# Kernel optimization log

Hardware: AMD Instinct MI355X
Metric: run time of the kernel (lower is better)

## Reference

```python
import jax, jax.numpy as jnp
import numpy as np

H = 1024   # hidden_size
V = 32000  # output_size (vocab)
B = 64     # batch
S = 2048   # encoder seq_len


def setup_inputs() -> dict:
    key = jax.random.key(0)
    ks = jax.random.split(key, 12)
    sc = 0.02
    return {
        "input_seq": jax.random.randint(ks[0], (B,), 0, V),
        "last_hidden": jax.random.normal(ks[1], (1, B, H), jnp.float32),
        "encoder_outputs": jax.random.normal(ks[2], (S, B, H), jnp.float32),
        "emb": jax.random.normal(ks[3], (V, H), jnp.float32) * sc,
        "w_ih": jax.random.normal(ks[4], (3 * H, H), jnp.float32) * sc,
        "w_hh": jax.random.normal(ks[5], (3 * H, H), jnp.float32) * sc,
        "b_ih": jnp.zeros((3 * H,), jnp.float32),
        "b_hh": jnp.zeros((3 * H,), jnp.float32),
        "attn_w": jax.random.normal(ks[6], (H, H), jnp.float32) * sc,
        "attn_b": jnp.zeros((H,), jnp.float32),
        "concat_w": jax.random.normal(ks[7], (H, 2 * H), jnp.float32) * sc,
        "concat_b": jnp.zeros((H,), jnp.float32),
        "out_w": jax.random.normal(ks[8], (V, H), jnp.float32) * sc,
        "out_b": jnp.zeros((V,), jnp.float32),
    }


def _forward(input_seq, last_hidden, encoder_outputs, emb, w_ih, w_hh, b_ih, b_hh,
             attn_w, attn_b, concat_w, concat_b, out_w, out_b):
    # 1. embedding (dropout = identity in eval)
    x = emb[input_seq]                      # [b, h]
    h = last_hidden[0]                      # [b, h]
    # 2. single-step GRU (PyTorch gate order: reset, update, new)
    gx = x @ w_ih.T + b_ih                  # [b, 3h]
    gh = h @ w_hh.T + b_hh                  # [b, 3h]
    r = jax.nn.sigmoid(gx[:, :H] + gh[:, :H])
    z = jax.nn.sigmoid(gx[:, H:2 * H] + gh[:, H:2 * H])
    n = jnp.tanh(gx[:, 2 * H:] + r * gh[:, 2 * H:])
    h_new = (1.0 - z) * n + z * h           # [b, h] = rnn_output
    # 3. Luong 'general' attention: score = y . (W enc + b)
    proj = jnp.einsum('sbh,gh->sbg', encoder_outputs, attn_w) + attn_b  # [s,b,h]
    scores = jnp.einsum('bh,sbh->bs', h_new, proj)                      # [b,s]
    attn_weights = jax.nn.softmax(scores, axis=-1)                      # [b,s]
    # 4. context = weights bmm encoder_outputs
    context = jnp.einsum('bs,sbh->bh', attn_weights, encoder_outputs)   # [b,h]
    # 5. concat -> linear -> tanh -> out
    cat = jnp.concatenate([h_new, context], axis=-1)                    # [b,2h]
    concat_output = jnp.tanh(cat @ concat_w.T + concat_b)               # [b,h]
    output = concat_output @ out_w.T + out_b                            # [b,V]
    return output, h_new[None], attn_weights[:, None, :]


def reference(input_seq, last_hidden, encoder_outputs, emb, w_ih, w_hh, b_ih, b_hh,
              attn_w, attn_b, concat_w, concat_b, out_w, out_b):
    return _forward(input_seq, last_hidden, encoder_outputs, emb, w_ih, w_hh, b_ih,
                    b_hh, attn_w, attn_b, concat_w, concat_b, out_w, out_b)
```

## Files before the change

kernel.cpp:

```cpp
#include <hip/hip_runtime.h>

#define HS 1024
#define VS 32000
#define BS 64
#define SS 2048
#define NCH 64
#define SCH (SS/NCH)

typedef __attribute__((ext_vector_type(4))) float f4v;
typedef __attribute__((ext_vector_type(8))) short s8v;

__device__ __forceinline__ float sigmf(float x) { return 1.0f / (1.0f + __expf(-x)); }

__device__ __forceinline__ short bf16c(float f) {
  unsigned u = __builtin_bit_cast(unsigned, f);
  u = (u + 0x7FFFu + ((u >> 16) & 1u)) >> 16;
  return (short)u;
}

__global__ __launch_bounds__(256) void k_prep(const int* __restrict__ idx,
    const float* __restrict__ emb, const float* __restrict__ hid,
    const float* __restrict__ aw,
    short* __restrict__ fx, short* __restrict__ fh, short* __restrict__ awf) {
  int t = blockIdx.x * 256 + threadIdx.x;
  {
    int lane = t & 63, nt = (t >> 6) & 63, kt = t >> 12;
    int kr = kt * 32 + ((lane >> 4) & 3) * 8;
    int col = nt * 16 + (lane & 15);
    const float* sp = aw + (size_t)kr * HS + col;
    s8v v;
#pragma unroll
    for (int j = 0; j < 8; j++) v[j] = bf16c(sp[(size_t)j * HS]);
    *(s8v*)(awf + (size_t)t * 8) = v;
  }
  if (t < 8192) {
    int lane = t & 63, ct = (t >> 6) & 3, kt = t >> 8;
    int col = ct * 16 + (lane & 15);
    int kr = kt * 32 + ((lane >> 4) & 3) * 8;
    const float* sp = emb + (size_t)idx[col] * HS + kr;
    s8v v;
#pragma unroll
    for (int j = 0; j < 8; j++) v[j] = bf16c(sp[j]);
    *(s8v*)(fx + (size_t)t * 8) = v;
  } else if (t < 16384) {
    int t2 = t - 8192;
    int lane = t2 & 63, ct = (t2 >> 6) & 3, kt = t2 >> 8;
    int col = ct * 16 + (lane & 15);
    int kr = kt * 32 + ((lane >> 4) & 3) * 8;
    const float* sp = hid + (size_t)col * HS + kr;
    s8v v;
#pragma unroll
    for (int j = 0; j < 8; j++) v[j] = bf16c(sp[j]);
    *(s8v*)(fh + (size_t)t2 * 8) = v;
  }
}

template<int K, int OL>
__global__ __launch_bounds__(256) void mfsk(
    const float* __restrict__ W0, const short* __restrict__ xf0,
    const float* __restrict__ bias0, void* __restrict__ dst0,
    const float* __restrict__ W1, const short* __restrict__ xf1,
    const float* __restrict__ bias1, void* __restrict__ dst1) {
  const float* W    = blockIdx.y ? W1 : W0;
  const short* xf   = blockIdx.y ? xf1 : xf0;
  const float* bias = blockIdx.y ? bias1 : bias0;
  void* dst         = blockIdx.y ? dst1 : dst0;
  int lane = threadIdx.x & 63;
  int ks = threadIdx.x >> 6;
  int mt = blockIdx.x;
  int row = mt * 16 + (lane & 15);
  const int KW = (K / 32) / 4;
  const float* wp = W + (size_t)row * K + ((lane >> 4) * 8);
  const s8v* xp = (const s8v*)xf + lane;
  f4v acc0 = {0,0,0,0}, acc1 = {0,0,0,0}, acc2 = {0,0,0,0}, acc3 = {0,0,0,0};
#pragma unroll 4
  for (int kk = 0; kk < KW; kk++) {
    int kt = ks * KW + kk;
    float4 wa = *(const float4*)(wp + (size_t)kt * 32);
    float4 wb = *(const float4*)(wp + (size_t)kt * 32 + 4);
    s8v a;
    a[0] = bf16c(wa.x); a[1] = bf16c(wa.y); a[2] = bf16c(wa.z); a[3] = bf16c(wa.w);
    a[4] = bf16c(wb.x); a[5] = bf16c(wb.y); a[6] = bf16c(wb.z); a[7] = bf16c(wb.w);
    const s8v* xk = xp + (size_t)kt * 256;
    acc0 = __builtin_amdgcn_mfma_f32_16x16x32_bf16(a, xk[0],   acc0, 0, 0, 0);
    acc1 = __builtin_amdgcn_mfma_f32_16x16x32_bf16(a, xk[64],  acc1, 0, 0, 0);
    acc2 = __builtin_amdgcn_mfma_f32_16x16x32_bf16(a, xk[128], acc2, 0, 0, 0);
    acc3 = __builtin_amdgcn_mfma_f32_16x16x32_bf16(a, xk[192], acc3, 0, 0, 0);
  }
  __shared__ float red[4][4][4][64];
#pragma unroll
  for (int r = 0; r < 4; r++) {
    red[ks][0][r][lane] = acc0[r];
    red[ks][1][r][lane] = acc1[r];
    red[ks][2][r][lane] = acc2[r];
    red[ks][3][r][lane] = acc3[r];
  }
  __syncthreads();
  int ct = ks;
  int rr0 = mt * 16 + (lane >> 4) * 4;
  int col = ct * 16 + (lane & 15);
#pragma unroll
  for (int r = 0; r < 4; r++) {
    float v = red[0][ct][r][lane] + red[1][ct][r][lane] +
              red[2][ct][r][lane] + red[3][ct][r][lane] + bias[rr0 + r];
    if (OL == 0)
      ((float*)dst)[(size_t)(rr0 + r) * BS + col] = v;
    else
      ((short*)dst)[(size_t)col * HS + rr0 + r] = bf16c(tanhf(v));
  }
}

__global__ __launch_bounds__(256) void k_hnew(const float* __restrict__ gxt,
    const float* __restrict__ ght, const float* __restrict__ hid,
    float* __restrict__ out_h, short* __restrict__ fcat) {
  int tid = blockIdx.x * 256 + threadIdx.x;
  int b = tid & 63, i = tid >> 6;
  float r = sigmf(gxt[i * BS + b] + ght[i * BS + b]);
  float z = sigmf(gxt[(HS + i) * BS + b] + ght[(HS + i) * BS + b]);
  float n = tanhf(gxt[(2 * HS + i) * BS + b] + r * ght[(2 * HS + i) * BS + b]);
  float hn = (1.0f - z) * n + z * hid[(size_t)b * HS + i];
  out_h[(size_t)b * HS + i] = hn;
  int kt = i >> 5, j = i & 7;
  int lane = (b & 15) | (((i >> 3) & 3) << 4);
  int ct = b >> 4;
  fcat[((size_t)((kt * 4 + ct) * 64 + lane)) * 8 + j] = bf16c(hn);
}

__global__ __launch_bounds__(256) void k_qgemm(const float* __restrict__ hnr,
    const short* __restrict__ awf, float* __restrict__ qrow) {
  int lane = threadIdx.x & 63;
  int mt = threadIdx.x >> 6;
  int nt = blockIdx.x;
  const float* ap = hnr + (size_t)(mt * 16 + (lane & 15)) * HS + ((lane >> 4) * 8);
  const s8v* bp = (const s8v*)awf + (size_t)nt * 64 + lane;
  f4v acc = {0,0,0,0};
#pragma unroll 4
  for (int kt = 0; kt < 32; kt++) {
    float4 wa = *(const float4*)(ap + kt * 32);
    float4 wb = *(const float4*)(ap + kt * 32 + 4);
    s8v a;
    a[0] = bf16c(wa.x); a[1] = bf16c(wa.y); a[2] = bf16c(wa.z); a[3] = bf16c(wa.w);
    a[4] = bf16c(wb.x); a[5] = bf16c(wb.y); a[6] = bf16c(wb.z); a[7] = bf16c(wb.w);
    acc = __builtin_amdgcn_mfma_f32_16x16x32_bf16(a, bp[(size_t)kt * 4096], acc, 0, 0, 0);
  }
  int r0 = mt * 16 + (lane >> 4) * 4;
  int hcol = nt * 16 + (lane & 15);
#pragma unroll
  for (int r = 0; r < 4; r++)
    qrow[(size_t)(r0 + r) * HS + hcol] = acc[r];
}

__global__ __launch_bounds__(256, 4) void k_attn(const float* __restrict__ enc,
    const float* __restrict__ qrow, float* __restrict__ scores,
    float* __restrict__ mch, float* __restrict__ lch, float* __restrict__ ctxp) {
  int lane = threadIdx.x & 63;
  int w = blockIdx.x * 4 + (threadIdx.x >> 6);
  int b = w & 63;
  int ch = w >> 6;
  const float* qb = qrow + (size_t)b * HS + lane * 4;
  float4 q0 = *(const float4*)(qb + 0);
  float4 q1 = *(const float4*)(qb + 256);
  float4 q2 = *(const float4*)(qb + 512);
  float4 q3 = *(const float4*)(qb + 768);
  int s0 = ch * SCH;
  const float* ep = enc + ((size_t)s0 * BS + b) * HS + lane * 4;
  float4 e0 = *(const float4*)(ep + 0);
  float4 e1 = *(const float4*)(ep + 256);
  float4 e2 = *(const float4*)(ep + 512);
  float4 e3 = *(const float4*)(ep + 768);
  float m = -1e30f, l = 0.f;
  float4 a0 = {0,0,0,0}, a1 = {0,0,0,0}, a2 = {0,0,0,0}, a3 = {0,0,0,0};
  for (int si = 0; si < SCH; si++) {
    float4 c0 = e0, c1 = e1, c2 = e2, c3 = e3;
    if (si + 1 < SCH) {
      const float* np = ep + (size_t)BS * HS;
      e0 = *(const float4*)(np + 0);
      e1 = *(const float4*)(np + 256);
      e2 = *(const float4*)(np + 512);
      e3 = *(const float4*)(np + 768);
    }
    ep += (size_t)BS * HS;
    float d0 = fmaf(c0.x,q0.x, fmaf(c0.y,q0.y, fmaf(c0.z,q0.z, c0.w*q0.w)));
    float d1 = fmaf(c1.x,q1.x, fmaf(c1.y,q1.y, fmaf(c1.z,q1.z, c1.w*q1.w)));
    float d2 = fmaf(c2.x,q2.x, fmaf(c2.y,q2.y, fmaf(c2.z,q2.z, c2.w*q2.w)));
    float d3 = fmaf(c3.x,q3.x, fmaf(c3.y,q3.y, fmaf(c3.z,q3.z, c3.w*q3.w)));
    float p = (d0 + d1) + (d2 + d3);
#pragma unroll
    for (int off = 32; off; off >>= 1) p += __shfl_xor(p, off, 64);
    if (lane == 0) scores[(size_t)b * SS + s0 + si] = p;
    float mn = fmaxf(m, p);
    float sc = __expf(m - mn);
    float pr = __expf(p - mn);
    l = fmaf(l, sc, pr);
    a0.x = fmaf(a0.x, sc, pr * c0.x); a0.y = fmaf(a0.y, sc, pr * c0.y);
    a0.z = fmaf(a0.z, sc, pr * c0.z); a0.w = fmaf(a0.w, sc, pr * c0.w);
    a1.x = fmaf(a1.x, sc, pr * c1.x); a1.y = fmaf(a1.y, sc, pr * c1.y);
    a1.z = fmaf(a1.z, sc, pr * c1.z); a1.w = fmaf(a1.w, sc, pr * c1.w);
    a2.x = fmaf(a2.x, sc, pr * c2.x); a2.y = fmaf(a2.y, sc, pr * c2.y);
    a2.z = fmaf(a2.z, sc, pr * c2.z); a2.w = fmaf(a2.w, sc, pr * c2.w);
    a3.x = fmaf(a3.x, sc, pr * c3.x); a3.y = fmaf(a3.y, sc, pr * c3.y);
    a3.z = fmaf(a3.z, sc, pr * c3.z); a3.w = fmaf(a3.w, sc, pr * c3.w);
    m = mn;
  }
  if (lane == 0) { mch[b * NCH + ch] = m; lch[b * NCH + ch] = l; }
  float* cp = ctxp + ((size_t)(b * NCH + ch)) * HS + lane * 4;
  *(float4*)(cp + 0)   = a0;
  *(float4*)(cp + 256) = a1;
  *(float4*)(cp + 512) = a2;
  *(float4*)(cp + 768) = a3;
}

__global__ __launch_bounds__(256) void k_combine(const float* __restrict__ mch,
    const float* __restrict__ lch, const float* __restrict__ ctxp,
    const float* __restrict__ scores, short* __restrict__ fcat,
    float* __restrict__ wout) {
  int b = blockIdx.x;
  int t = threadIdx.x;
  __shared__ float sm[NCH], sl[NCH], ssc[NCH];
  if (t < NCH) { sm[t] = mch[b * NCH + t]; sl[t] = lch[b * NCH + t]; }
  __syncthreads();
  float mstar = -1e30f;
  for (int c = 0; c < NCH; c++) mstar = fmaxf(mstar, sm[c]);
  if (t < NCH) ssc[t] = __expf(sm[t] - mstar);
  __syncthreads();
  float L = 0.f;
  for (int c = 0; c < NCH; c++) L = fmaf(sl[c], ssc[c], L);
  float invL = 1.0f / L;
  int h = blockIdx.y * 256 + t;
  float acc = 0.f;
  for (int c = 0; c < NCH; c++)
    acc = fmaf(ctxp[((size_t)(b * NCH + c)) * HS + h], ssc[c], acc);
  float ctx = acc * invL;
  int kc = HS + h;
  int kt = kc >> 5, j = kc & 7;
  int lane2 = (b & 15) | (((kc >> 3) & 3) << 4);
  int ct = b >> 4;
  fcat[((size_t)((kt * 4 + ct) * 64 + lane2)) * 8 + j] = bf16c(ctx);
  if (blockIdx.y == 0)
    for (int s = t; s < SS; s += 256)
      wout[(size_t)b * SS + s] = __expf(scores[(size_t)b * SS + s] - mstar) * invL;
}

__global__ __launch_bounds__(256) void k_out2(const short* __restrict__ cbf,
    const float* __restrict__ ow, const float* __restrict__ ob,
    float* __restrict__ out0) {
  int lane = threadIdx.x & 63;
  int wv = threadIdx.x >> 6;
  int nt = blockIdx.x * 4 + wv;
  int v0 = nt * 16;
  const float* wp = ow + (size_t)(v0 + (lane & 15)) * HS + ((lane >> 4) * 8);
  const short* a0p = cbf + (size_t)(0  + (lane & 15)) * HS + ((lane >> 4) * 8);
  const short* a1p = a0p + (size_t)16 * HS;
  const short* a2p = a0p + (size_t)32 * HS;
  const short* a3p = a0p + (size_t)48 * HS;
  f4v acc0 = {0,0,0,0}, acc1 = {0,0,0,0}, acc2 = {0,0,0,0}, acc3 = {0,0,0,0};
#pragma unroll 4
  for (int kt = 0; kt < 32; kt++) {
    float4 wa = *(const float4*)(wp + kt * 32);
    float4 wb = *(const float4*)(wp + kt * 32 + 4);
    s8v bf;
    bf[0] = bf16c(wa.x); bf[1] = bf16c(wa.y); bf[2] = bf16c(wa.z); bf[3] = bf16c(wa.w);
    bf[4] = bf16c(wb.x); bf[5] = bf16c(wb.y); bf[6] = bf16c(wb.z); bf[7] = bf16c(wb.w);
    s8v fa0 = *(const s8v*)(a0p + kt * 32);
    s8v fa1 = *(const s8v*)(a1p + kt * 32);
    s8v fa2 = *(const s8v*)(a2p + kt * 32);
    s8v fa3 = *(const s8v*)(a3p + kt * 32);
    acc0 = __builtin_amdgcn_mfma_f32_16x16x32_bf16(fa0, bf, acc0, 0, 0, 0);
    acc1 = __builtin_amdgcn_mfma_f32_16x16x32_bf16(fa1, bf, acc1, 0, 0, 0);
    acc2 = __builtin_amdgcn_mfma_f32_16x16x32_bf16(fa2, bf, acc2, 0, 0, 0);
    acc3 = __builtin_amdgcn_mfma_f32_16x16x32_bf16(fa3, bf, acc3, 0, 0, 0);
  }
  float bv = ob[v0 + (lane & 15)];
  int rb = (lane >> 4) * 4;
  int vc = v0 + (lane & 15);
#pragma unroll
  for (int r = 0; r < 4; r++) {
    out0[(size_t)(0  + rb + r) * VS + vc] = acc0[r] + bv;
    out0[(size_t)(16 + rb + r) * VS + vc] = acc1[r] + bv;
    out0[(size_t)(32 + rb + r) * VS + vc] = acc2[r] + bv;
    out0[(size_t)(48 + rb + r) * VS + vc] = acc3[r] + bv;
  }
}

extern "C" void kernel_launch(void* const* d_in, const int* in_sizes, int n_in,
                              void* d_out, int out_size, void* d_ws, size_t ws_size,
                              hipStream_t stream) {
  const int*   idx  = (const int*)d_in[0];
  const float* hid  = (const float*)d_in[1];
  const float* enc  = (const float*)d_in[2];
  const float* emb  = (const float*)d_in[3];
  const float* w_ih = (const float*)d_in[4];
  const float* w_hh = (const float*)d_in[5];
  const float* b_ih = (const float*)d_in[6];
  const float* b_hh = (const float*)d_in[7];
  const float* aw   = (const float*)d_in[8];
  const float* cw   = (const float*)d_in[10];
  const float* cb   = (const float*)d_in[11];
  const float* ow   = (const float*)d_in[12];
  const float* ob   = (const float*)d_in[13];

  float* out0  = (float*)d_out;
  float* out_h = out0 + (size_t)BS * VS;
  float* out_w = out_h + (size_t)BS * HS;

  float* ws   = (float*)d_ws;
  float* gxt  = ws;
  float* ght  = gxt + (size_t)3 * HS * BS;
  float* qrow = ght + (size_t)3 * HS * BS;
  float* scr  = qrow + (size_t)HS * BS;
  float* mch  = scr + (size_t)BS * SS;
  float* lch  = mch + (size_t)BS * NCH;
  float* ctxp = lch + (size_t)BS * NCH;
  short* awf  = (short*)(ctxp + (size_t)BS * NCH * HS);
  short* fx   = awf + (size_t)HS * HS;
  short* fh   = fx  + (size_t)HS * BS;
  short* fcat = fh  + (size_t)HS * BS;
  short* cbf  = fcat + (size_t)2 * HS * BS;

  k_prep   <<<dim3(512), dim3(256), 0, stream>>>(idx, emb, hid, aw, fx, fh, awf);
  mfsk<HS, 0><<<dim3(3 * HS / 16, 2), dim3(256), 0, stream>>>(
      w_ih, fx, b_ih, gxt, w_hh, fh, b_hh, ght);
  k_hnew   <<<dim3(HS * BS / 256), dim3(256), 0, stream>>>(gxt, ght, hid, out_h, fcat);
  k_qgemm  <<<dim3(HS / 16), dim3(256), 0, stream>>>(out_h, awf, qrow);
  k_attn   <<<dim3(BS * NCH / 4), dim3(256), 0, stream>>>(enc, qrow, scr, mch, lch, ctxp);
  k_combine<<<dim3(BS, 4), dim3(256), 0, stream>>>(mch, lch, ctxp, scr, fcat, out_w);
  mfsk<2 * HS, 1><<<dim3(HS / 16, 1), dim3(256), 0, stream>>>(
      cw, fcat, cb, cbf, cw, fcat, cb, cbf);
  k_out2   <<<dim3(VS / 64), dim3(256), 0, stream>>>(cbf, ow, ob, out0);
}
```

Before: 210.4 us.

## Fuse prep conversion into GRU gate GEMM, drop awf pre-pack, double-buffer attention loads

Removes the k_prep kernel. The GRU gate GEMM now gathers embedding and hidden rows directly and converts them to bf16 in-register, summing the K-split partials through shared memory. k_qgemm reads the fp32 attention weight with strided column loads instead of a pre-packed bf16 layout. The attention loop keeps two encoder rows in flight to deepen prefetch. This saves one launch and the pack traffic, at the cost of redundant conversions and poorly coalesced strided loads in k_qgemm.

```diff
diff --git a/kernel.cpp b/kernel.cpp
--- a/kernel.cpp
+++ b/kernel.cpp
@@ -18,53 +18,80 @@
   return (short)u;
 }
 
-__global__ __launch_bounds__(256) void k_prep(const int* __restrict__ idx,
-    const float* __restrict__ emb, const float* __restrict__ hid,
-    const float* __restrict__ aw,
-    short* __restrict__ fx, short* __restrict__ fh, short* __restrict__ awf) {
-  int t = blockIdx.x * 256 + threadIdx.x;
-  {
-    int lane = t & 63, nt = (t >> 6) & 63, kt = t >> 12;
-    int kr = kt * 32 + ((lane >> 4) & 3) * 8;
-    int col = nt * 16 + (lane & 15);
-    const float* sp = aw + (size_t)kr * HS + col;
-    s8v v;
-#pragma unroll
-    for (int j = 0; j < 8; j++) v[j] = bf16c(sp[(size_t)j * HS]);
-    *(s8v*)(awf + (size_t)t * 8) = v;
-  }
-  if (t < 8192) {
-    int lane = t & 63, ct = (t >> 6) & 3, kt = t >> 8;
+__global__ __launch_bounds__(256) void k_gatesf(
+    const int* __restrict__ idx, const float* __restrict__ emb,
+    const float* __restrict__ hid,
+    const float* __restrict__ w_ih, const float* __restrict__ w_hh,
+    const float* __restrict__ b_ih, const float* __restrict__ b_hh,
+    float* __restrict__ gxt, float* __restrict__ ght) {
+  int y = blockIdx.y;
+  const float* W    = y ? w_hh : w_ih;
+  const float* bias = y ? b_hh : b_ih;
+  float* dst        = y ? ght : gxt;
+  int lane = threadIdx.x & 63;
+  int ks = threadIdx.x >> 6;
+  int mt = blockIdx.x;
+  int row = mt * 16 + (lane & 15);
+  const float* wp = W + (size_t)row * HS + ((lane >> 4) * 8);
+  const float* rp[4];
+#pragma unroll
+  for (int ct = 0; ct < 4; ct++) {
     int col = ct * 16 + (lane & 15);
-    int kr = kt * 32 + ((lane >> 4) & 3) * 8;
-    const float* sp = emb + (size_t)idx[col] * HS + kr;
-    s8v v;
-#pragma unroll
-    for (int j = 0; j < 8; j++) v[j] = bf16c(sp[j]);
-    *(s8v*)(fx + (size_t)t * 8) = v;
-  } else if (t < 16384) {
-    int t2 = t - 8192;
-    int lane = t2 & 63, ct = (t2 >> 6) & 3, kt = t2 >> 8;
-    int col = ct * 16 + (lane & 15);
-    int kr = kt * 32 + ((lane >> 4) & 3) * 8;
-    const float* sp = hid + (size_t)col * HS + kr;
-    s8v v;
-#pragma unroll
-    for (int j = 0; j < 8; j++) v[j] = bf16c(sp[j]);
-    *(s8v*)(fh + (size_t)t2 * 8) = v;
+    rp[ct] = y ? (hid + (size_t)col * HS) : (emb + (size_t)idx[col] * HS);
+  }
+  f4v acc0 = {0,0,0,0}, acc1 = {0,0,0,0}, acc2 = {0,0,0,0}, acc3 = {0,0,0,0};
+#pragma unroll 4
+  for (int kk = 0; kk < 8; kk++) {
+    int kt = ks * 8 + kk;
+    int kr = kt * 32 + ((lane >> 4) * 8);
+    float4 wa = *(const float4*)(wp + (size_t)kt * 32);
+    float4 wb = *(const float4*)(wp + (size_t)kt * 32 + 4);
+    s8v a;
+    a[0] = bf16c(wa.x); a[1] = bf16c(wa.y); a[2] = bf16c(wa.z); a[3] = bf16c(wa.w);
+    a[4] = bf16c(wb.x); a[5] = bf16c(wb.y); a[6] = bf16c(wb.z); a[7] = bf16c(wb.w);
+    float4 xa, xb;
+    s8v bf;
+    xa = *(const float4*)(rp[0] + kr); xb = *(const float4*)(rp[0] + kr + 4);
+    bf[0] = bf16c(xa.x); bf[1] = bf16c(xa.y); bf[2] = bf16c(xa.z); bf[3] = bf16c(xa.w);
+    bf[4] = bf16c(xb.x); bf[5] = bf16c(xb.y); bf[6] = bf16c(xb.z); bf[7] = bf16c(xb.w);
+    acc0 = __builtin_amdgcn_mfma_f32_16x16x32_bf16(a, bf, acc0, 0, 0, 0);
+    xa = *(const float4*)(rp[1] + kr); xb = *(const float4*)(rp[1] + kr + 4);
+    bf[0] = bf16c(xa.x); bf[1] = bf16c(xa.y); bf[2] = bf16c(xa.z); bf[3] = bf16c(xa.w);
+    bf[4] = bf16c(xb.x); bf[5] = bf16c(xb.y); bf[6] = bf16c(xb.z); bf[7] = bf16c(xb.w);
+    acc1 = __builtin_amdgcn_mfma_f32_16x16x32_bf16(a, bf, acc1, 0, 0, 0);
+    xa = *(const float4*)(rp[2] + kr); xb = *(const float4*)(rp[2] + kr + 4);
+    bf[0] = bf16c(xa.x); bf[1] = bf16c(xa.y); bf[2] = bf16c(xa.z); bf[3] = bf16c(xa.w);
+    bf[4] = bf16c(xb.x); bf[5] = bf16c(xb.y); bf[6] = bf16c(xb.z); bf[7] = bf16c(xb.w);
+    acc2 = __builtin_amdgcn_mfma_f32_16x16x32_bf16(a, bf, acc2, 0, 0, 0);
+    xa = *(const float4*)(rp[3] + kr); xb = *(const float4*)(rp[3] + kr + 4);
+    bf[0] = bf16c(xa.x); bf[1] = bf16c(xa.y); bf[2] = bf16c(xa.z); bf[3] = bf16c(xa.w);
+    bf[4] = bf16c(xb.x); bf[5] = bf16c(xb.y); bf[6] = bf16c(xb.z); bf[7] = bf16c(xb.w);
+    acc3 = __builtin_amdgcn_mfma_f32_16x16x32_bf16(a, bf, acc3, 0, 0, 0);
+  }
+  __shared__ float red[4][4][4][64];
+#pragma unroll
+  for (int r = 0; r < 4; r++) {
+    red[ks][0][r][lane] = acc0[r];
+    red[ks][1][r][lane] = acc1[r];
+    red[ks][2][r][lane] = acc2[r];
+    red[ks][3][r][lane] = acc3[r];
+  }
+  __syncthreads();
+  int ct = ks;
+  int rr0 = mt * 16 + (lane >> 4) * 4;
+  int col = ct * 16 + (lane & 15);
+#pragma unroll
+  for (int r = 0; r < 4; r++) {
+    float v = red[0][ct][r][lane] + red[1][ct][r][lane] +
+              red[2][ct][r][lane] + red[3][ct][r][lane] + bias[rr0 + r];
+    dst[(size_t)(rr0 + r) * BS + col] = v;
   }
 }
 
 template<int K, int OL>
 __global__ __launch_bounds__(256) void mfsk(
-    const float* __restrict__ W0, const short* __restrict__ xf0,
-    const float* __restrict__ bias0, void* __restrict__ dst0,
-    const float* __restrict__ W1, const short* __restrict__ xf1,
-    const float* __restrict__ bias1, void* __restrict__ dst1) {
-  const float* W    = blockIdx.y ? W1 : W0;
-  const short* xf   = blockIdx.y ? xf1 : xf0;
-  const float* bias = blockIdx.y ? bias1 : bias0;
-  void* dst         = blockIdx.y ? dst1 : dst0;
+    const float* __restrict__ W, const short* __restrict__ xf,
+    const float* __restrict__ bias, void* __restrict__ dst) {
   int lane = threadIdx.x & 63;
   int ks = threadIdx.x >> 6;
   int mt = blockIdx.x;
@@ -127,12 +154,12 @@
 }
 
 __global__ __launch_bounds__(256) void k_qgemm(const float* __restrict__ hnr,
-    const short* __restrict__ awf, float* __restrict__ qrow) {
+    const float* __restrict__ aw, float* __restrict__ qrow) {
   int lane = threadIdx.x & 63;
   int mt = threadIdx.x >> 6;
   int nt = blockIdx.x;
   const float* ap = hnr + (size_t)(mt * 16 + (lane & 15)) * HS + ((lane >> 4) * 8);
-  const s8v* bp = (const s8v*)awf + (size_t)nt * 64 + lane;
+  const float* awc = aw + nt * 16 + (lane & 15);
   f4v acc = {0,0,0,0};
 #pragma unroll 4
   for (int kt = 0; kt < 32; kt++) {
@@ -141,7 +168,12 @@
     s8v a;
     a[0] = bf16c(wa.x); a[1] = bf16c(wa.y); a[2] = bf16c(wa.z); a[3] = bf16c(wa.w);
     a[4] = bf16c(wb.x); a[5] = bf16c(wb.y); a[6] = bf16c(wb.z); a[7] = bf16c(wb.w);
-    acc = __builtin_amdgcn_mfma_f32_16x16x32_bf16(a, bp[(size_t)kt * 4096], acc, 0, 0, 0);
+    int kr = kt * 32 + ((lane >> 4) * 8);
+    const float* bp = awc + (size_t)kr * HS;
+    s8v bfr;
+#pragma unroll
+    for (int j = 0; j < 8; j++) bfr[j] = bf16c(bp[(size_t)j * HS]);
+    acc = __builtin_amdgcn_mfma_f32_16x16x32_bf16(a, bfr, acc, 0, 0, 0);
   }
   int r0 = mt * 16 + (lane >> 4) * 4;
   int hcol = nt * 16 + (lane & 15);
@@ -163,44 +195,82 @@
   float4 q2 = *(const float4*)(qb + 512);
   float4 q3 = *(const float4*)(qb + 768);
   int s0 = ch * SCH;
+  const size_t sstr = (size_t)BS * HS;
   const float* ep = enc + ((size_t)s0 * BS + b) * HS + lane * 4;
-  float4 e0 = *(const float4*)(ep + 0);
-  float4 e1 = *(const float4*)(ep + 256);
-  float4 e2 = *(const float4*)(ep + 512);
-  float4 e3 = *(const float4*)(ep + 768);
+  float4 eA0 = *(const float4*)(ep + 0);
+  float4 eA1 = *(const float4*)(ep + 256);
+  float4 eA2 = *(const float4*)(ep + 512);
+  float4 eA3 = *(const float4*)(ep + 768);
+  const float* ep1 = ep + sstr;
+  float4 eB0 = *(const float4*)(ep1 + 0);
+  float4 eB1 = *(const float4*)(ep1 + 256);
+  float4 eB2 = *(const float4*)(ep1 + 512);
+  float4 eB3 = *(const float4*)(ep1 + 768);
   float m = -1e30f, l = 0.f;
   float4 a0 = {0,0,0,0}, a1 = {0,0,0,0}, a2 = {0,0,0,0}, a3 = {0,0,0,0};
-  for (int si = 0; si < SCH; si++) {
-    float4 c0 = e0, c1 = e1, c2 = e2, c3 = e3;
-    if (si + 1 < SCH) {
-      const float* np = ep + (size_t)BS * HS;
-      e0 = *(const float4*)(np + 0);
-      e1 = *(const float4*)(np + 256);
-      e2 = *(const float4*)(np + 512);
-      e3 = *(const float4*)(np + 768);
+  for (int si = 0; si < SCH; si += 2) {
+    {
+      float4 c0 = eA0, c1 = eA1, c2 = eA2, c3 = eA3;
+      if (si + 2 < SCH) {
+        const float* np = ep + (size_t)(si + 2) * sstr;
+        eA0 = *(const float4*)(np + 0);
+        eA1 = *(const float4*)(np + 256);
+        eA2 = *(const float4*)(np + 512);
+        eA3 = *(const float4*)(np + 768);
+      }
+      float d0 = fmaf(c0.x,q0.x, fmaf(c0.y,q0.y, fmaf(c0.z,q0.z, c0.w*q0.w)));
+      float d1 = fmaf(c1.x,q1.x, fmaf(c1.y,q1.y, fmaf(c1.z,q1.z, c1.w*q1.w)));
+      float d2 = fmaf(c2.x,q2.x, fmaf(c2.y,q2.y, fmaf(c2.z,q2.z, c2.w*q2.w)));
+      float d3 = fmaf(c3.x,q3.x, fmaf(c3.y,q3.y, fmaf(c3.z,q3.z, c3.w*q3.w)));
+      float p = (d0 + d1) + (d2 + d3);
+#pragma unroll
+      for (int off = 32; off; off >>= 1) p += __shfl_xor(p, off, 64);
+      if (lane == 0) scores[(size_t)b * SS + s0 + si] = p;
+      float mn = fmaxf(m, p);
+      float sc = __expf(m - mn);
+      float pr = __expf(p - mn);
+      l = fmaf(l, sc, pr);
+      a0.x = fmaf(a0.x, sc, pr * c0.x); a0.y = fmaf(a0.y, sc, pr * c0.y);
+      a0.z = fmaf(a0.z, sc, pr * c0.z); a0.w = fmaf(a0.w, sc, pr * c0.w);
+      a1.x = fmaf(a1.x, sc, pr * c1.x); a1.y = fmaf(a1.y, sc, pr * c1.y);
+      a1.z = fmaf(a1.z, sc, pr * c1.z); a1.w = fmaf(a1.w, sc, pr * c1.w);
+      a2.x = fmaf(a2.x, sc, pr * c2.x); a2.y = fmaf(a2.y, sc, pr * c2.y);
+      a2.z = fmaf(a2.z, sc, pr * c2.z); a2.w = fmaf(a2.w, sc, pr * c2.w);
+      a3.x = fmaf(a3.x, sc, pr * c3.x); a3.y = fmaf(a3.y, sc, pr * c3.y);
+      a3.z = fmaf(a3.z, sc, pr * c3.z); a3.w = fmaf(a3.w, sc, pr * c3.w);
+      m = mn;
     }
-    ep += (size_t)BS * HS;
-    float d0 = fmaf(c0.x,q0.x, fmaf(c0.y,q0.y, fmaf(c0.z,q0.z, c0.w*q0.w)));
-    float d1 = fmaf(c1.x,q1.x, fmaf(c1.y,q1.y, fmaf(c1.z,q1.z, c1.w*q1.w)));
-    float d2 = fmaf(c2.x,q2.x, fmaf(c2.y,q2.y, fmaf(c2.z,q2.z, c2.w*q2.w)));
-    float d3 = fmaf(c3.x,q3.x, fmaf(c3.y,q3.y, fmaf(c3.z,q3.z, c3.w*q3.w)));
-    float p = (d0 + d1) + (d2 + d3);
-#pragma unroll
-    for (int off = 32; off; off >>= 1) p += __shfl_xor(p, off, 64);
-    if (lane == 0) scores[(size_t)b * SS + s0 + si] = p;
-    float mn = fmaxf(m, p);
-    float sc = __expf(m - mn);
-    float pr = __expf(p - mn);
-    l = fmaf(l, sc, pr);
-    a0.x = fmaf(a0.x, sc, pr * c0.x); a0.y = fmaf(a0.y, sc, pr * c0.y);
-    a0.z = fmaf(a0.z, sc, pr * c0.z); a0.w = fmaf(a0.w, sc, pr * c0.w);
-    a1.x = fmaf(a1.x, sc, pr * c1.x); a1.y = fmaf(a1.y, sc, pr * c1.y);
-    a1.z = fmaf(a1.z, sc, pr * c1.z); a1.w = fmaf(a1.w, sc, pr * c1.w);
-    a2.x = fmaf(a2.x, sc, pr * c2.x); a2.y = fmaf(a2.y, sc, pr * c2.y);
-    a2.z = fmaf(a2.z, sc, pr * c2.z); a2.w = fmaf(a2.w, sc, pr * c2.w);
-    a3.x = fmaf(a3.x, sc, pr * c3.x); a3.y = fmaf(a3.y, sc, pr * c3.y);
-    a3.z = fmaf(a3.z, sc, pr * c3.z); a3.w = fmaf(a3.w, sc, pr * c3.w);
-    m = mn;
+    {
+      float4 c0 = eB0, c1 = eB1, c2 = eB2, c3 = eB3;
+      if (si + 3 < SCH) {
+        const float* np = ep + (size_t)(si + 3) * sstr;
+        eB0 = *(const float4*)(np + 0);
+        eB1 = *(const float4*)(np + 256);
+        eB2 = *(const float4*)(np + 512);
+        eB3 = *(const float4*)(np + 768);
+      }
+      float d0 = fmaf(c0.x,q0.x, fmaf(c0.y,q0.y, fmaf(c0.z,q0.z, c0.w*q0.w)));
+      float d1 = fmaf(c1.x,q1.x, fmaf(c1.y,q1.y, fmaf(c1.z,q1.z, c1.w*q1.w)));
+      float d2 = fmaf(c2.x,q2.x, fmaf(c2.y,q2.y, fmaf(c2.z,q2.z, c2.w*q2.w)));
+      float d3 = fmaf(c3.x,q3.x, fmaf(c3.y,q3.y, fmaf(c3.z,q3.z, c3.w*q3.w)));
+      float p = (d0 + d1) + (d2 + d3);
+#pragma unroll
+      for (int off = 32; off; off >>= 1) p += __shfl_xor(p, off, 64);
+      if (lane == 0) scores[(size_t)b * SS + s0 + si + 1] = p;
+      float mn = fmaxf(m, p);
+      float sc = __expf(m - mn);
+      float pr = __expf(p - mn);
+      l = fmaf(l, sc, pr);
+      a0.x = fmaf(a0.x, sc, pr * c0.x); a0.y = fmaf(a0.y, sc, pr * c0.y);
+      a0.z = fmaf(a0.z, sc, pr * c0.z); a0.w = fmaf(a0.w, sc, pr * c0.w);
+      a1.x = fmaf(a1.x, sc, pr * c1.x); a1.y = fmaf(a1.y, sc, pr * c1.y);
+      a1.z = fmaf(a1.z, sc, pr * c1.z); a1.w = fmaf(a1.w, sc, pr * c1.w);
+      a2.x = fmaf(a2.x, sc, pr * c2.x); a2.y = fmaf(a2.y, sc, pr * c2.y);
+      a2.z = fmaf(a2.z, sc, pr * c2.z); a2.w = fmaf(a2.w, sc, pr * c2.w);
+      a3.x = fmaf(a3.x, sc, pr * c3.x); a3.y = fmaf(a3.y, sc, pr * c3.y);
+      a3.z = fmaf(a3.z, sc, pr * c3.z); a3.w = fmaf(a3.w, sc, pr * c3.w);
+      m = mn;
+    }
   }
   if (lane == 0) { mch[b * NCH + ch] = m; lch[b * NCH + ch] = l; }
   float* cp = ctxp + ((size_t)(b * NCH + ch)) * HS + lane * 4;
@@ -311,20 +381,15 @@
   float* mch  = scr + (size_t)BS * SS;
   float* lch  = mch + (size_t)BS * NCH;
   float* ctxp = lch + (size_t)BS * NCH;
-  short* awf  = (short*)(ctxp + (size_t)BS * NCH * HS);
-  short* fx   = awf + (size_t)HS * HS;
-  short* fh   = fx  + (size_t)HS * BS;
-  short* fcat = fh  + (size_t)HS * BS;
+  short* fcat = (short*)(ctxp + (size_t)BS * NCH * HS);
   short* cbf  = fcat + (size_t)2 * HS * BS;
 
-  k_prep   <<<dim3(512), dim3(256), 0, stream>>>(idx, emb, hid, aw, fx, fh, awf);
-  mfsk<HS, 0><<<dim3(3 * HS / 16, 2), dim3(256), 0, stream>>>(
-      w_ih, fx, b_ih, gxt, w_hh, fh, b_hh, ght);
+  k_gatesf <<<dim3(3 * HS / 16, 2), dim3(256), 0, stream>>>(
+      idx, emb, hid, w_ih, w_hh, b_ih, b_hh, gxt, ght);
   k_hnew   <<<dim3(HS * BS / 256), dim3(256), 0, stream>>>(gxt, ght, hid, out_h, fcat);
-  k_qgemm  <<<dim3(HS / 16), dim3(256), 0, stream>>>(out_h, awf, qrow);
+  k_qgemm  <<<dim3(HS / 16), dim3(256), 0, stream>>>(out_h, aw, qrow);
   k_attn   <<<dim3(BS * NCH / 4), dim3(256), 0, stream>>>(enc, qrow, scr, mch, lch, ctxp);
   k_combine<<<dim3(BS, 4), dim3(256), 0, stream>>>(mch, lch, ctxp, scr, fcat, out_w);
-  mfsk<2 * HS, 1><<<dim3(HS / 16, 1), dim3(256), 0, stream>>>(
-      cw, fcat, cb, cbf, cw, fcat, cb, cbf);
+  mfsk<2 * HS, 1><<<dim3(HS / 16), dim3(256), 0, stream>>>(cw, fcat, cb, cbf);
   k_out2   <<<dim3(VS / 64), dim3(256), 0, stream>>>(cbf, ow, ob, out0);
 }
```

Measured after the change: 224.6 us. +6.7%, slower.
